# Performance work log

Measured on AMD Instinct MI355X. Metric: run time of the kernel, lower is better.

Reference implementation:

```python
import jax, jax.numpy as jnp
import numpy as np

THETA = 1.2
XI = 0.3


def setup_inputs() -> dict:
    key = jax.random.key(0)
    k1, k2 = jax.random.split(key)
    B, D = 8192, 512
    x = jax.random.normal(k1, (B, D), dtype=jnp.float32)
    y = jax.random.randint(k2, (B,), 0, 1000, dtype=jnp.int64)
    return {"x": x, "y": y}


def reference(x, y):
    B = x.shape[0]
    # per-sample L2 normalization: n_i = x_i / ||x_i||
    n = x / jnp.linalg.norm(x, axis=1, keepdims=True)  # [B, D]
    # pairwise squared distances ||n_i - n_j||^2 = |n_i|^2 + |n_j|^2 - 2 n_i.n_j
    sq = jnp.sum(n * n, axis=1)                        # [B]
    G = n @ n.T                                        # [B, B]
    dist2 = sq[:, None] + sq[None, :] - 2.0 * G        # [B, B]
    # indicator: +1 if same label else -1 (symmetric)
    ind = jnp.where(y[:, None] == y[None, :], 1.0, -1.0)
    # original loops i in [0,B), j in [i,B): upper triangle including diagonal
    idx = jnp.arange(B)
    mask = (idx[None, :] >= idx[:, None]).astype(x.dtype)
    hinge = jnp.maximum(THETA - dist2, 0.0)
    total = jnp.sum(mask * (XI + ind * hinge))
    m_scalar = 1.0 / (B * B - B)
    return m_scalar * total
```

## Files before the change

### kernel.cpp

```cpp
#include <hip/hip_runtime.h>
#include <cstdint>
#include <cstddef>

#define THETA 1.2f
#define XI 0.3f
#define BDIM 8192
#define DDIM 512
#define NTILE 64
#define NUPPER 2080
#define GRID 512
#define NPAIRS_UP (((double)BDIM * (double)(BDIM + 1)) * 0.5)

typedef float f32x4 __attribute__((ext_vector_type(4)));
typedef int i32x8 __attribute__((ext_vector_type(8)));

__global__ __launch_bounds__(256) void normalize_rows(
    const float* __restrict__ x, unsigned char* __restrict__ nf8,
    float* __restrict__ sq, unsigned int* __restrict__ counter)
{
    if (blockIdx.x == 0 && threadIdx.x == 0) { *counter = 0u; }
    int row = blockIdx.x * 4 + (threadIdx.x >> 6);
    int l = threadIdx.x & 63;
    const float4* xr = (const float4*)(x + (size_t)row * DDIM);
    float4 f0 = xr[l];
    float4 f1 = xr[l + 64];
    float s = f0.x*f0.x + f0.y*f0.y + f0.z*f0.z + f0.w*f0.w
            + f1.x*f1.x + f1.y*f1.y + f1.z*f1.z + f1.w*f1.w;
    #pragma unroll
    for (int m = 1; m < 64; m <<= 1) s += __shfl_xor(s, m);
    float rn = rsqrtf(s);
    int pk0 = __builtin_amdgcn_cvt_pk_fp8_f32(f0.x * rn, f0.y * rn, 0, false);
    pk0     = __builtin_amdgcn_cvt_pk_fp8_f32(f0.z * rn, f0.w * rn, pk0, true);
    int pk1 = __builtin_amdgcn_cvt_pk_fp8_f32(f1.x * rn, f1.y * rn, 0, false);
    pk1     = __builtin_amdgcn_cvt_pk_fp8_f32(f1.z * rn, f1.w * rn, pk1, true);
    int* rowp = (int*)(nf8 + (size_t)row * DDIM);
    rowp[l] = pk0;
    rowp[l + 64] = pk1;
    if (l == 0) sq[row] = s * rn * rn;
}

__device__ __forceinline__ void decode_tile(int u, int& ti, int& tj) {
    int t = (int)((sqrtf(8.0f * (float)u + 1.0f) - 1.0f) * 0.5f);
    while ((t + 1) * (t + 2) / 2 <= u) ++t;
    while (t * (t + 1) / 2 > u) --t;
    tj = t;
    ti = u - t * (t + 1) / 2;
}

__global__ __launch_bounds__(256, 2) void gram_hinge(
    const unsigned char* __restrict__ nf8, const float* __restrict__ sq,
    const int* __restrict__ y, double* __restrict__ part,
    unsigned int* __restrict__ counter, float* __restrict__ out)
{
    __shared__ unsigned char As[2][128 * 128];
    __shared__ unsigned char Bs[2][128 * 128];
    __shared__ float wpart[4];
    __shared__ double dpart[4];
    __shared__ int is_last;

    int tid = threadIdx.x;
    int w = tid >> 6, l = tid & 63;
    int wr = w >> 1, wc = w & 1;
    int lr = l & 15, q = l >> 4;

    int srow = l >> 3;
    int sgran = (l & 7) ^ srow;
    int sm = lr & 7;

    auto stage = [&](unsigned char* dAb, unsigned char* dBb, int pti, int ptj, int pc) {
        const unsigned char* gA = nf8
            + ((size_t)(pti * 128 + w * 32 + srow)) * DDIM + pc * 128 + sgran * 16;
        const unsigned char* gB = nf8
            + ((size_t)(ptj * 128 + w * 32 + srow)) * DDIM + pc * 128 + sgran * 16;
        unsigned char* dA = dAb + (w * 32) * 128;
        unsigned char* dB = dBb + (w * 32) * 128;
        #pragma unroll
        for (int i = 0; i < 4; ++i) {
            __builtin_amdgcn_global_load_lds(
                (const __attribute__((address_space(1))) void*)(gA + (size_t)i * 8 * DDIM),
                (__attribute__((address_space(3))) void*)(dA + i * 1024), 16, 0, 0);
            __builtin_amdgcn_global_load_lds(
                (const __attribute__((address_space(1))) void*)(gB + (size_t)i * 8 * DDIM),
                (__attribute__((address_space(3))) void*)(dB + i * 1024), 16, 0, 0);
        }
    };

    float acc0 = 0.f, acc1 = 0.f, acc2 = 0.f, acc3 = 0.f;

    int u = blockIdx.x;
    int ti, tj;
    decode_tile(u, ti, tj);

    stage(As[0], Bs[0], ti, tj, 0);

    while (u < NUPPER) {
        int u_next = u + GRID;
        bool have_next = (u_next < NUPPER);
        int ti_n = 0, tj_n = 0;
        if (have_next) decode_tile(u_next, ti_n, tj_n);

        f32x4 accv[4][4] = {};

        #pragma unroll 1
        for (int c = 0; c < 4; ++c) {
            if (c < 3) {
                stage(As[(c + 1) & 1], Bs[(c + 1) & 1], ti, tj, c + 1);
                asm volatile("s_waitcnt vmcnt(8)" ::: "memory");
            } else if (have_next) {
                stage(As[0], Bs[0], ti_n, tj_n, 0);
                asm volatile("s_waitcnt vmcnt(8)" ::: "memory");
            } else {
                asm volatile("s_waitcnt vmcnt(0)" ::: "memory");
            }
            asm volatile("s_barrier" ::: "memory");

            const unsigned char* Ab = As[c & 1];
            const unsigned char* Bb = Bs[c & 1];
            i32x8 bf[4];
            #pragma unroll
            for (int f = 0; f < 4; ++f) {
                int rB = (wc * 64 + f * 16 + lr) * 128;
                int4 b0 = *(const int4*)(Bb + rB + (((2 * q + 0) ^ sm) << 4));
                int4 b1 = *(const int4*)(Bb + rB + (((2 * q + 1) ^ sm) << 4));
                bf[f][0] = b0.x; bf[f][1] = b0.y; bf[f][2] = b0.z; bf[f][3] = b0.w;
                bf[f][4] = b1.x; bf[f][5] = b1.y; bf[f][6] = b1.z; bf[f][7] = b1.w;
            }
            __builtin_amdgcn_s_setprio(1);
            #pragma unroll
            for (int mi = 0; mi < 4; ++mi) {
                int rA = (wr * 64 + mi * 16 + lr) * 128;
                int4 a0 = *(const int4*)(Ab + rA + (((2 * q + 0) ^ sm) << 4));
                int4 a1 = *(const int4*)(Ab + rA + (((2 * q + 1) ^ sm) << 4));
                i32x8 af;
                af[0] = a0.x; af[1] = a0.y; af[2] = a0.z; af[3] = a0.w;
                af[4] = a1.x; af[5] = a1.y; af[6] = a1.z; af[7] = a1.w;
                #pragma unroll
                for (int ni = 0; ni < 4; ++ni)
                    accv[mi][ni] = __builtin_amdgcn_mfma_scale_f32_16x16x128_f8f6f4(
                        af, bf[ni], accv[mi][ni],
                        0, 0, 0, 0x7F7F7F7F, 0, 0x7F7F7F7F);
            }
            __builtin_amdgcn_s_setprio(0);

            asm volatile("s_barrier" ::: "memory");
        }

        {
            int jb = tj * 128 + wc * 64 + lr;
            float sqj[4]; int yj[4];
            #pragma unroll
            for (int ni = 0; ni < 4; ++ni) {
                sqj[ni] = sq[jb + ni * 16];
                yj[ni]  = y[jb + ni * 16];
            }
            bool skip = (ti == tj) && (wr > wc);
            bool full = (ti != tj) || (wc > wr);
            if (!skip) {
                if (full) {
                    #pragma unroll
                    for (int mi = 0; mi < 4; ++mi) {
                        #pragma unroll
                        for (int r = 0; r < 4; ++r) {
                            int ia = ti * 128 + wr * 64 + mi * 16 + q * 4 + r;
                            float ci = THETA - sq[ia];
                            int yi = y[ia];
                            float h0 = fmaxf(fmaf(2.f, accv[mi][0][r], ci - sqj[0]), 0.f);
                            acc0 += (yi == yj[0]) ? h0 : -h0;
                            float h1 = fmaxf(fmaf(2.f, accv[mi][1][r], ci - sqj[1]), 0.f);
                            acc1 += (yi == yj[1]) ? h1 : -h1;
                            float h2 = fmaxf(fmaf(2.f, accv[mi][2][r], ci - sqj[2]), 0.f);
                            acc2 += (yi == yj[2]) ? h2 : -h2;
                            float h3 = fmaxf(fmaf(2.f, accv[mi][3][r], ci - sqj[3]), 0.f);
                            acc3 += (yi == yj[3]) ? h3 : -h3;
                        }
                    }
                } else {
                    #pragma unroll
                    for (int mi = 0; mi < 4; ++mi) {
                        #pragma unroll
                        for (int r = 0; r < 4; ++r) {
                            int rl_ = mi * 16 + q * 4 + r;
                            int ia = ti * 128 + wr * 64 + rl_;
                            float ci = THETA - sq[ia];
                            int yi = y[ia];
                            #pragma unroll
                            for (int ni = 0; ni < 4; ++ni) {
                                float h = fmaxf(fmaf(2.f, accv[mi][ni][r], ci - sqj[ni]), 0.f);
                                float sh = (yi == yj[ni]) ? h : -h;
                                if (ni * 16 + lr >= rl_) acc0 += sh;
                            }
                        }
                    }
                }
            }
        }

        u = u_next; ti = ti_n; tj = tj_n;
    }

    float local = (acc0 + acc1) + (acc2 + acc3);
    #pragma unroll
    for (int off = 32; off > 0; off >>= 1) local += __shfl_down(local, off);
    if (l == 0) wpart[w] = local;
    __syncthreads();
    if (tid == 0) {
        double ssum = (double)wpart[0] + (double)wpart[1]
                    + (double)wpart[2] + (double)wpart[3];
        __hip_atomic_store(&part[blockIdx.x], ssum, __ATOMIC_RELEASE, __HIP_MEMORY_SCOPE_AGENT);
        unsigned int ticket = __hip_atomic_fetch_add(
            counter, 1u, __ATOMIC_ACQ_REL, __HIP_MEMORY_SCOPE_AGENT);
        is_last = (ticket == GRID - 1) ? 1 : 0;
    }
    __syncthreads();
    if (is_last) {
        double s = 0.0;
        for (int i = tid; i < GRID; i += 256)
            s += __hip_atomic_load(&part[i], __ATOMIC_ACQUIRE, __HIP_MEMORY_SCOPE_AGENT);
        #pragma unroll
        for (int off = 32; off > 0; off >>= 1) s += __shfl_down(s, off);
        if (l == 0) dpart[w] = s;
        __syncthreads();
        if (tid == 0) {
            double total = (dpart[0] + dpart[1] + dpart[2] + dpart[3])
                         + (double)XI * NPAIRS_UP;
            const double m = 1.0 / ((double)BDIM * (double)BDIM - (double)BDIM);
            out[0] = (float)(total * m);
        }
    }
}

extern "C" void kernel_launch(void* const* d_in, const int* in_sizes, int n_in,
                              void* d_out, int out_size, void* d_ws, size_t ws_size,
                              hipStream_t stream) {
    const float* x = (const float*)d_in[0];
    const int* y = (const int*)d_in[1];
    float* out = (float*)d_out;

    unsigned char* nf8 = (unsigned char*)d_ws;
    char* p = (char*)d_ws + (size_t)BDIM * DDIM;
    float* sq = (float*)p;
    unsigned int* counter = (unsigned int*)(p + (size_t)BDIM * 4);
    double* part = (double*)(p + (size_t)BDIM * 4 + 64);

    normalize_rows<<<BDIM / 4, 256, 0, stream>>>(x, nf8, sq, counter);
    gram_hinge<<<GRID, 256, 0, stream>>>(nf8, sq, y, part, counter, out);
}
```

Before: 103.4 us.

## Store fp8 rows in MFMA fragment layout and load B directly from global

The normalize kernel now writes fp8 data pre-arranged into 16-row by 128-k fragment blocks, so each lane's 32-byte MFMA operand is contiguous. The gram kernel keeps only the A tile in LDS, loading it with linear global_load_lds copies, and reads B fragments straight from global memory into registers, halving LDS use. This allows occupancy to rise to 3 blocks per CU, and the grid doubles to 1024. The trade-off is that B reads now go through the cache hierarchy each k-step rather than being shared through LDS, and the vmcnt wait counts were retuned to match. Removing the XOR swizzle depends on the new layout producing conflict-free LDS reads.

```diff
diff --git a/kernel.cpp b/kernel.cpp
--- a/kernel.cpp
+++ b/kernel.cpp
@@ -8,11 +8,12 @@
 #define DDIM 512
 #define NTILE 64
 #define NUPPER 2080
-#define GRID 512
+#define GRID 1024
 #define NPAIRS_UP (((double)BDIM * (double)(BDIM + 1)) * 0.5)
 
 typedef float f32x4 __attribute__((ext_vector_type(4)));
 typedef int i32x8 __attribute__((ext_vector_type(8)));
+
 
 __global__ __launch_bounds__(256) void normalize_rows(
     const float* __restrict__ x, unsigned char* __restrict__ nf8,
@@ -33,9 +34,12 @@
     pk0     = __builtin_amdgcn_cvt_pk_fp8_f32(f0.z * rn, f0.w * rn, pk0, true);
     int pk1 = __builtin_amdgcn_cvt_pk_fp8_f32(f1.x * rn, f1.y * rn, 0, false);
     pk1     = __builtin_amdgcn_cvt_pk_fp8_f32(f1.z * rn, f1.w * rn, pk1, true);
-    int* rowp = (int*)(nf8 + (size_t)row * DDIM);
-    rowp[l] = pk0;
-    rowp[l + 64] = pk1;
+    size_t base = (size_t)(row >> 4) * 4 * 2048;
+    int within = ((row & 15) + ((l >> 3) & 3) * 16) * 32 + (l & 7) * 4;
+    int kc0 = l >> 5;
+    int kc1 = (l >> 5) + 2;
+    *(int*)(nf8 + base + (size_t)kc0 * 2048 + within) = pk0;
+    *(int*)(nf8 + base + (size_t)kc1 * 2048 + within) = pk1;
     if (l == 0) sq[row] = s * rn * rn;
 }
 
@@ -47,13 +51,12 @@
     ti = u - t * (t + 1) / 2;
 }
 
-__global__ __launch_bounds__(256, 2) void gram_hinge(
+__global__ __launch_bounds__(256, 3) void gram_hinge(
     const unsigned char* __restrict__ nf8, const float* __restrict__ sq,
     const int* __restrict__ y, double* __restrict__ part,
     unsigned int* __restrict__ counter, float* __restrict__ out)
 {
-    __shared__ unsigned char As[2][128 * 128];
-    __shared__ unsigned char Bs[2][128 * 128];
+    __shared__ unsigned char As[2][16384];
     __shared__ float wpart[4];
     __shared__ double dpart[4];
     __shared__ int is_last;
@@ -63,25 +66,16 @@
     int wr = w >> 1, wc = w & 1;
     int lr = l & 15, q = l >> 4;
 
-    int srow = l >> 3;
-    int sgran = (l & 7) ^ srow;
-    int sm = lr & 7;
-
-    auto stage = [&](unsigned char* dAb, unsigned char* dBb, int pti, int ptj, int pc) {
-        const unsigned char* gA = nf8
-            + ((size_t)(pti * 128 + w * 32 + srow)) * DDIM + pc * 128 + sgran * 16;
-        const unsigned char* gB = nf8
-            + ((size_t)(ptj * 128 + w * 32 + srow)) * DDIM + pc * 128 + sgran * 16;
-        unsigned char* dA = dAb + (w * 32) * 128;
-        unsigned char* dB = dBb + (w * 32) * 128;
+    auto stageA = [&](unsigned char* dAb, int pti, int pc) {
         #pragma unroll
         for (int i = 0; i < 4; ++i) {
+            int t = w * 4 + i;
+            int rf = t >> 1, half = t & 1;
+            const unsigned char* src = nf8
+                + ((size_t)((pti * 8 + rf) * 4 + pc)) * 2048 + half * 1024 + l * 16;
             __builtin_amdgcn_global_load_lds(
-                (const __attribute__((address_space(1))) void*)(gA + (size_t)i * 8 * DDIM),
-                (__attribute__((address_space(3))) void*)(dA + i * 1024), 16, 0, 0);
-            __builtin_amdgcn_global_load_lds(
-                (const __attribute__((address_space(1))) void*)(gB + (size_t)i * 8 * DDIM),
-                (__attribute__((address_space(3))) void*)(dB + i * 1024), 16, 0, 0);
+                (const __attribute__((address_space(1))) void*)src,
+                (__attribute__((address_space(3))) void*)(dAb + t * 1024), 16, 0, 0);
         }
     };
 
@@ -91,7 +85,7 @@
     int ti, tj;
     decode_tile(u, ti, tj);
 
-    stage(As[0], Bs[0], ti, tj, 0);
+    stageA(As[0], ti, 0);
 
     while (u < NUPPER) {
         int u_next = u + GRID;
@@ -103,37 +97,29 @@
 
         #pragma unroll 1
         for (int c = 0; c < 4; ++c) {
-            if (c < 3) {
-                stage(As[(c + 1) & 1], Bs[(c + 1) & 1], ti, tj, c + 1);
-                asm volatile("s_waitcnt vmcnt(8)" ::: "memory");
-            } else if (have_next) {
-                stage(As[0], Bs[0], ti_n, tj_n, 0);
-                asm volatile("s_waitcnt vmcnt(8)" ::: "memory");
-            } else {
-                asm volatile("s_waitcnt vmcnt(0)" ::: "memory");
-            }
-            asm volatile("s_barrier" ::: "memory");
-
-            const unsigned char* Ab = As[c & 1];
-            const unsigned char* Bb = Bs[c & 1];
             i32x8 bf[4];
             #pragma unroll
-            for (int f = 0; f < 4; ++f) {
-                int rB = (wc * 64 + f * 16 + lr) * 128;
-                int4 b0 = *(const int4*)(Bb + rB + (((2 * q + 0) ^ sm) << 4));
-                int4 b1 = *(const int4*)(Bb + rB + (((2 * q + 1) ^ sm) << 4));
-                bf[f][0] = b0.x; bf[f][1] = b0.y; bf[f][2] = b0.z; bf[f][3] = b0.w;
-                bf[f][4] = b1.x; bf[f][5] = b1.y; bf[f][6] = b1.z; bf[f][7] = b1.w;
-            }
+            for (int ni = 0; ni < 4; ++ni)
+                bf[ni] = *(const i32x8*)(nf8
+                    + ((size_t)((tj * 8 + wc * 4 + ni) * 4 + c)) * 2048 + l * 32);
+            __builtin_amdgcn_sched_barrier(0);
+
+            if (c < 3) {
+                stageA(As[(c + 1) & 1], ti, c + 1);
+                asm volatile("s_waitcnt vmcnt(12)" ::: "memory");
+            } else if (have_next) {
+                stageA(As[0], ti_n, 0);
+                asm volatile("s_waitcnt vmcnt(12)" ::: "memory");
+            } else {
+                asm volatile("s_waitcnt vmcnt(8)" ::: "memory");
+            }
+            asm volatile("s_barrier" ::: "memory");
+
+            const unsigned char* Ab = As[c & 1];
             __builtin_amdgcn_s_setprio(1);
             #pragma unroll
             for (int mi = 0; mi < 4; ++mi) {
-                int rA = (wr * 64 + mi * 16 + lr) * 128;
-                int4 a0 = *(const int4*)(Ab + rA + (((2 * q + 0) ^ sm) << 4));
-                int4 a1 = *(const int4*)(Ab + rA + (((2 * q + 1) ^ sm) << 4));
-                i32x8 af;
-                af[0] = a0.x; af[1] = a0.y; af[2] = a0.z; af[3] = a0.w;
-                af[4] = a1.x; af[5] = a1.y; af[6] = a1.z; af[7] = a1.w;
+                i32x8 af = *(const i32x8*)(Ab + (wr * 4 + mi) * 2048 + l * 32);
                 #pragma unroll
                 for (int ni = 0; ni < 4; ++ni)
                     accv[mi][ni] = __builtin_amdgcn_mfma_scale_f32_16x16x128_f8f6f4(
```

Result: slower. 120.4 us (+16.4%).
